# Kernel tuning notes

Hardware: AMD Instinct MI355X
Metric: run time of the kernel (lower is better)

## Reference

```python
import jax, jax.numpy as jnp
import numpy as np

D_MODEL = 2048
N_HEADS = 16
HEAD_DIM = D_MODEL // N_HEADS
BATCH = 2
SEQ = 2048


def rotate_half(x):
    x1, x2 = jnp.split(x, 2, axis=-1)
    return jnp.concatenate((-x2, x1), axis=-1)


def rope_emb(seq_len, head_dim, dtype=jnp.float32):
    inv_freq = 1.0 / (10000.0 ** (jnp.arange(0, head_dim, 2, dtype=jnp.float32) / head_dim))
    t = jnp.arange(seq_len, dtype=jnp.float32)
    freqs = jnp.einsum('i,j->ij', t, inv_freq)            # [S, D/2]
    emb = jnp.concatenate((freqs, freqs), axis=-1)        # [S, D]
    return emb[None, :, None, :].astype(dtype)            # [1, S, 1, D]


def apply_rope(x, emb):
    return x * jnp.cos(emb) + rotate_half(x) * jnp.sin(emb)


def setup_inputs() -> dict:
    key = jax.random.key(0)
    ks = jax.random.split(key, 5)
    s = 1.0 / np.sqrt(D_MODEL)
    return {
        'query': jax.random.normal(ks[0], (BATCH, SEQ, D_MODEL), jnp.float32),
        'Wq': jax.random.normal(ks[1], (D_MODEL, D_MODEL), jnp.float32) * s,
        'Wk': jax.random.normal(ks[2], (D_MODEL, D_MODEL), jnp.float32) * s,
        'Wv': jax.random.normal(ks[3], (D_MODEL, D_MODEL), jnp.float32) * s,
        'Wo': jax.random.normal(ks[4], (D_MODEL, D_MODEL), jnp.float32) * s,
    }


def reference(query, Wq, Wk, Wv, Wo):
    B, S, _ = query.shape
    # QKV projections (nn.Linear: x @ W.T), reshape to [B, S, H, Dh]
    q = (query @ Wq.T).reshape(B, S, N_HEADS, HEAD_DIM)
    k = (query @ Wk.T).reshape(B, S, N_HEADS, HEAD_DIM)
    v = (query @ Wv.T).reshape(B, S, N_HEADS, HEAD_DIM)
    emb = rope_emb(S, HEAD_DIM, q.dtype)
    q = apply_rope(q, emb)
    k = apply_rope(k, emb)
    # causal SDPA
    scale = HEAD_DIM ** -0.5
    scores = jnp.einsum('bqhd,bkhd->bhqk', q, k) * scale  # [B, H, S, S]
    causal = jnp.tril(jnp.ones((S, S), dtype=bool))
    scores = jnp.where(causal, scores, jnp.finfo(scores.dtype).min)
    attn = jax.nn.softmax(scores, axis=-1)
    out = jnp.einsum('bhqk,bkhd->bqhd', attn, v).reshape(B, S, D_MODEL)
    return out @ Wo.T
```

## Files before the change

kernel.cpp:

```cpp
#include <hip/hip_runtime.h>
#include <math.h>

#define BATCH 2
#define SEQ 2048
#define DMODEL 2048
#define NHEADS 16
#define HEADDIM 128
#define MTOT (BATCH * SEQ)
#define QKVLD 6144

typedef __attribute__((ext_vector_type(8))) _Float16 half8;
typedef __attribute__((ext_vector_type(4))) _Float16 half4;
typedef __attribute__((ext_vector_type(4))) float f32x4;

__device__ __forceinline__ void gl_lds16(const void* g, void* l) {
    __builtin_amdgcn_global_load_lds(
        (const __attribute__((address_space(1))) unsigned int*)g,
        (__attribute__((address_space(3))) unsigned int*)l, 16, 0, 0);
}

__global__ __launch_bounds__(256) void f2h_conv(const float* __restrict__ src,
                                                _Float16* __restrict__ dst) {
    size_t i = ((size_t)blockIdx.x * 256 + threadIdx.x) * 8;
    float4 a = *(const float4*)(src + i);
    float4 b = *(const float4*)(src + i + 4);
    union { uint4 u; _Float16 h[8]; } o;
    o.h[0] = (_Float16)a.x; o.h[1] = (_Float16)a.y;
    o.h[2] = (_Float16)a.z; o.h[3] = (_Float16)a.w;
    o.h[4] = (_Float16)b.x; o.h[5] = (_Float16)b.y;
    o.h[6] = (_Float16)b.z; o.h[7] = (_Float16)b.w;
    *(uint4*)(dst + i) = o.u;
}

__global__ __launch_bounds__(256) void f2h3_conv(const float* __restrict__ s0,
                                                 const float* __restrict__ s1,
                                                 const float* __restrict__ s2,
                                                 _Float16* __restrict__ dst) {
    const float* src = (blockIdx.y == 0) ? s0 : (blockIdx.y == 1) ? s1 : s2;
    size_t i = ((size_t)blockIdx.x * 256 + threadIdx.x) * 8;
    float4 a = *(const float4*)(src + i);
    float4 b = *(const float4*)(src + i + 4);
    union { uint4 u; _Float16 h[8]; } o;
    o.h[0] = (_Float16)a.x; o.h[1] = (_Float16)a.y;
    o.h[2] = (_Float16)a.z; o.h[3] = (_Float16)a.w;
    o.h[4] = (_Float16)b.x; o.h[5] = (_Float16)b.y;
    o.h[6] = (_Float16)b.z; o.h[7] = (_Float16)b.w;
    *(uint4*)(dst + (size_t)blockIdx.y * (DMODEL * DMODEL) + i) = o.u;
}

#define SB0  __builtin_amdgcn_sched_barrier(0)
#define BAR  __builtin_amdgcn_s_barrier()
#define VMW4 do { SB0; asm volatile("s_waitcnt vmcnt(4)"); SB0; } while (0)
#define VMW0 do { SB0; asm volatile("s_waitcnt vmcnt(0)"); SB0; } while (0)

template <bool F16OUT>
__global__ __launch_bounds__(512, 2) void gemm8p(const _Float16* __restrict__ A,
                                                 const _Float16* __restrict__ W,
                                                 void* __restrict__ Cout,
                                                 int M, int N, int K) {
    __shared__ __align__(16) _Float16 LAb[2][2][128][64];
    __shared__ __align__(16) _Float16 LBb[2][2][128][64];

    const int tid = threadIdx.x;
    const int lane = tid & 63;
    const int wave = tid >> 6;
    const int quad = lane >> 4;
    const int lcol = lane & 15;
    const int wr = wave >> 2;
    const int wc = wave & 3;
    const int m0 = blockIdx.y * 256;
    const int n0 = blockIdx.x * 256;

    const int srow = tid >> 3;
    const int sc8p = tid & 7;
    const int sc8l = sc8p ^ (srow & 7);

#define STA(BUF, HALF, KT)                                                     \
    do {                                                                       \
        _Pragma("unroll") for (int j = 0; j < 2; j++)                          \
            gl_lds16(A + (size_t)(m0 + (HALF)*128 + j*64 + srow) * K +         \
                         (KT)*64 + sc8l*8,                                     \
                     &LAb[BUF][HALF][j*64 + srow][sc8p*8]);                    \
    } while (0)
#define STB(BUF, HALF, KT)                                                     \
    do {                                                                       \
        _Pragma("unroll") for (int j = 0; j < 2; j++)                          \
            gl_lds16(W + (size_t)(n0 + (HALF)*128 + j*64 + srow) * K +         \
                         (KT)*64 + sc8l*8,                                     \
                     &LBb[BUF][HALF][j*64 + srow][sc8p*8]);                    \
    } while (0)

    auto rdA = [&](int buf, int mf, int ks) -> half8 {
        int R = mf * 16 + lcol;
        return *(const half8*)&LAb[buf][wr][R]
                [(ks * 32 + quad * 8) ^ ((lcol & 7) << 3)];
    };
    auto rdB = [&](int buf, int nf, int ks) -> half8 {
        int R = (wc & 1) * 64 + nf * 16 + lcol;
        return *(const half8*)&LBb[buf][wc >> 1][R]
                [(ks * 32 + quad * 8) ^ ((lcol & 7) << 3)];
    };

    f32x4 acc[8][4];
#pragma unroll
    for (int i = 0; i < 8; i++)
#pragma unroll
        for (int j = 0; j < 4; j++) acc[i][j] = (f32x4){0.f, 0.f, 0.f, 0.f};

#define KTILE4(BUF, S1, S2, S3, S4, W4)                                        \
    {                                                                          \
        half8 a[4][2], b[4][2];                                                \
                         \
        _Pragma("unroll") for (int mf = 0; mf < 4; mf++)                       \
            _Pragma("unroll") for (int ks = 0; ks < 2; ks++)                   \
                a[mf][ks] = rdA(BUF, mf, ks);                                  \
        _Pragma("unroll") for (int nf = 0; nf < 2; nf++)                       \
            _Pragma("unroll") for (int ks = 0; ks < 2; ks++)                   \
                b[nf][ks] = rdB(BUF, nf, ks);                                  \
        S1; SB0; BAR; SB0;                                                     \
        __builtin_amdgcn_s_setprio(1);                                         \
        _Pragma("unroll") for (int ks = 0; ks < 2; ks++)                       \
            _Pragma("unroll") for (int mf = 0; mf < 4; mf++)                   \
                _Pragma("unroll") for (int nf = 0; nf < 2; nf++)               \
                    acc[mf][nf] = __builtin_amdgcn_mfma_f32_16x16x32_f16(      \
                        a[mf][ks], b[nf][ks], acc[mf][nf], 0, 0, 0);           \
        __builtin_amdgcn_s_setprio(0); SB0; BAR; SB0;                          \
                                             \
        _Pragma("unroll") for (int nf = 0; nf < 2; nf++)                       \
            _Pragma("unroll") for (int ks = 0; ks < 2; ks++)                   \
                b[2 + nf][ks] = rdB(BUF, 2 + nf, ks);                          \
        S2; SB0; BAR; SB0;                                                     \
        __builtin_amdgcn_s_setprio(1);                                         \
        _Pragma("unroll") for (int ks = 0; ks < 2; ks++)                       \
            _Pragma("unroll") for (int mf = 0; mf < 4; mf++)                   \
                _Pragma("unroll") for (int nf = 0; nf < 2; nf++)               \
                    acc[mf][2 + nf] = __builtin_amdgcn_mfma_f32_16x16x32_f16(  \
                        a[mf][ks], b[2 + nf][ks], acc[mf][2 + nf], 0, 0, 0);   \
        __builtin_amdgcn_s_setprio(0); SB0; BAR; SB0;                          \
               \
        _Pragma("unroll") for (int mf = 0; mf < 4; mf++)                       \
            _Pragma("unroll") for (int ks = 0; ks < 2; ks++)                   \
                a[mf][ks] = rdA(BUF, 4 + mf, ks);                              \
        S3; SB0; BAR; SB0;                                                     \
        __builtin_amdgcn_s_setprio(1);                                         \
        _Pragma("unroll") for (int ks = 0; ks < 2; ks++)                       \
            _Pragma("unroll") for (int mf = 0; mf < 4; mf++)                   \
                _Pragma("unroll") for (int nf = 0; nf < 2; nf++)               \
                    acc[4 + mf][nf] = __builtin_amdgcn_mfma_f32_16x16x32_f16(  \
                        a[mf][ks], b[nf][ks], acc[4 + mf][nf], 0, 0, 0);       \
        __builtin_amdgcn_s_setprio(0); SB0; BAR; SB0;                          \
              \
        S4; W4; BAR; SB0;                                                      \
        __builtin_amdgcn_s_setprio(1);                                         \
        _Pragma("unroll") for (int ks = 0; ks < 2; ks++)                       \
            _Pragma("unroll") for (int mf = 0; mf < 4; mf++)                   \
                _Pragma("unroll") for (int nf = 0; nf < 2; nf++)               \
                    acc[4 + mf][2 + nf] =                                      \
                        __builtin_amdgcn_mfma_f32_16x16x32_f16(                \
                            a[mf][ks], b[2 + nf][ks], acc[4 + mf][2 + nf],     \
                            0, 0, 0);                                          \
        __builtin_amdgcn_s_setprio(0); SB0; BAR; SB0;                          \
    }

    STB(0, 0, 0); STB(0, 1, 0); STA(0, 0, 0); STA(0, 1, 0);
    STB(1, 0, 1); STB(1, 1, 1);
    VMW4; BAR; SB0;

    const int niter = K >> 7;
    for (int i = 0; i < niter - 1; ++i) {
        const int t0 = 2 * i;
        KTILE4(0, STA(1, 0, t0 + 1), STA(1, 1, t0 + 1),
                  STB(0, 0, t0 + 2), STB(0, 1, t0 + 2), VMW4);
        KTILE4(1, STA(0, 0, t0 + 2), STA(0, 1, t0 + 2),
                  STB(1, 0, t0 + 3), STB(1, 1, t0 + 3), VMW4);
    }
    {
        const int t0 = 2 * (niter - 1);
        KTILE4(0, STA(1, 0, t0 + 1), STA(1, 1, t0 + 1),
                  (void)0, (void)0, VMW0);
        KTILE4(1, (void)0, (void)0, (void)0, (void)0, (void)0);
    }

    float* Cf = (float*)Cout;
    _Float16* Ch = (_Float16*)Cout;
#pragma unroll
    for (int mf = 0; mf < 8; mf++)
#pragma unroll
        for (int nf = 0; nf < 4; nf++)
#pragma unroll
            for (int r = 0; r < 4; r++) {
                size_t row = m0 + wr * 128 + mf * 16 + quad * 4 + r;
                size_t col = n0 + wc * 64 + nf * 16 + lcol;
                if (F16OUT)
                    Ch[row * N + col] = (_Float16)acc[mf][nf][r];
                else
                    Cf[row * N + col] = acc[mf][nf][r];
            }
#undef KTILE4
#undef STA
#undef STB
}

__global__ __launch_bounds__(256) void rope_qk(_Float16* __restrict__ buf) {
    size_t idx = (size_t)blockIdx.x * 256 + threadIdx.x;
    int d = (int)(idx & 63);
    int h = (int)((idx >> 6) & (NHEADS - 1));
    int qk = (int)((idx >> 10) & 1);
    int m = (int)(idx >> 11);
    int s = m & (SEQ - 1);
    float scale = qk ? 1.0f : 0.08838834764831845f;
    float inv = __expf(-(float)d * 0.14391156831212787f);
    float f = (float)s * inv;
    float sn, cs;
    __sincosf(f, &sn, &cs);
    size_t base = (size_t)m * QKVLD + qk * DMODEL + h * HEADDIM + d;
    float x1 = (float)buf[base];
    float x2 = (float)buf[base + 64];
    buf[base]      = (_Float16)((x1 * cs - x2 * sn) * scale);
    buf[base + 64] = (_Float16)((x2 * cs + x1 * sn) * scale);
}

__global__ __launch_bounds__(256) void conv_v_t(const _Float16* __restrict__ src,
                                                _Float16* __restrict__ dst) {
    __shared__ __align__(16) _Float16 T[32][72];
    const int tid = threadIdx.x;
    const int s0 = blockIdx.x * 64;
    const int d0 = blockIdx.y * 32;
    const int bh = blockIdx.z;
    const int b = bh >> 4;
    const int h = bh & 15;

    {
        int s = tid >> 2;
        int d8 = (tid & 3) * 8;
        union { uint4 u; _Float16 hh[8]; } v;
        v.u = *(const uint4*)(src + (size_t)(b * SEQ + s0 + s) * QKVLD +
                              2 * DMODEL + h * HEADDIM + d0 + d8);
#pragma unroll
        for (int j = 0; j < 8; j++) T[d8 + j][s] = v.hh[j];
    }
    __syncthreads();

    int row = tid >> 3;
    int chunk = tid & 7;
    uint4 val = *(const uint4*)&T[row][chunk * 8];
    *(uint4*)(dst + ((size_t)(bh * HEADDIM + d0 + row)) * SEQ + s0 + chunk * 8) = val;
}

__global__ __launch_bounds__(512) void attn_mfma(const _Float16* __restrict__ qkv,
                                                 const _Float16* __restrict__ vtb,
                                                 _Float16* __restrict__ ab) {
    __shared__ __align__(16) _Float16 Ks[64][136];
    __shared__ __align__(16) _Float16 Vts[128][72];
    __shared__ __align__(16) _Float16 Ps[8][16][72];

    const int tid = threadIdx.x;
    const int wave = tid >> 6;
    const int lane = tid & 63;
    const int quad = lane >> 4;
    const int lcol = lane & 15;

    const int h = blockIdx.y;
    const int b = blockIdx.z;
    const int qtA = blockIdx.x;

    const int kr0 = tid >> 4;
    const int ko0 = (tid & 15) * 8;
    const int vr0 = tid >> 3;
    const int vo0 = (tid & 7) * 8;

    const _Float16* kbp = qkv + (size_t)b * SEQ * QKVLD + DMODEL + h * HEADDIM;
    const _Float16* vbp = vtb + ((size_t)(b * NHEADS + h) * HEADDIM) * SEQ;

    uint4 kA, kB, vA, vB;
#define ISSUE_LOAD(kb)                                                        \
    do {                                                                      \
        int _kb = (kb);                                                       \
        kA = *(const uint4*)(kbp + (size_t)(_kb + kr0) * QKVLD + ko0);        \
        kB = *(const uint4*)(kbp + (size_t)(_kb + 32 + kr0) * QKVLD + ko0);   \
        vA = *(const uint4*)(vbp + (size_t)vr0 * SEQ + _kb + vo0);            \
        vB = *(const uint4*)(vbp + (size_t)(vr0 + 64) * SEQ + _kb + vo0);     \
    } while (0)

    ISSUE_LOAD(0);

    for (int ph = 0; ph < 2; ++ph) {
        const int qt = ph ? (15 - qtA) : qtA;
        const int q0 = qt * 128 + wave * 16;
        const int nkt = 2 * qt + 2;

        half8 aq[4];
        {
            const _Float16* qrow =
                qkv + (size_t)(b * SEQ + q0 + lcol) * QKVLD + h * HEADDIM;
#pragma unroll
            for (int st = 0; st < 4; st++)
                aq[st] = *(const half8*)(qrow + quad * 8 + 32 * st);
        }

        f32x4 Of[8];
#pragma unroll
        for (int dt = 0; dt < 8; dt++) Of[dt] = (f32x4){0.f, 0.f, 0.f, 0.f};
        float m_s = -1e30f, l_s = 0.f;

        for (int kt = 0; kt < nkt; ++kt) {
            const int kbase = kt << 6;

            __syncthreads();
            *(uint4*)&Ks[kr0][ko0]        = kA;
            *(uint4*)&Ks[kr0 + 32][ko0]   = kB;
            *(uint4*)&Vts[vr0][vo0]       = vA;
            *(uint4*)&Vts[vr0 + 64][vo0]  = vB;
            __syncthreads();

            if (kt + 1 < nkt)      ISSUE_LOAD((kt + 1) << 6);
            else if (ph == 0)      ISSUE_LOAD(0);

            if (kbase > q0 + 15) continue;

            f32x4 Sc[4];
#pragma unroll
            for (int s = 0; s < 4; s++) {
                Sc[s] = (f32x4){0.f, 0.f, 0.f, 0.f};
#pragma unroll
                for (int st = 0; st < 4; st++) {
                    half8 bk = *(const half8*)&Ks[16 * s + lcol][quad * 8 + 32 * st];
                    Sc[s] = __builtin_amdgcn_mfma_f32_16x16x32_f16(bk, aq[st], Sc[s],
                                                                   0, 0, 0);
                }
            }

            if (kbase + 63 > q0) {
#pragma unroll
                for (int s = 0; s < 4; s++)
#pragma unroll
                    for (int r = 0; r < 4; r++)
                        if (kbase + 16 * s + quad * 4 + r > q0 + lcol)
                            Sc[s][r] = -1e30f;
            }

            float pmax = Sc[0][0];
#pragma unroll
            for (int s = 0; s < 4; s++)
#pragma unroll
                for (int r = 0; r < 4; r++) pmax = fmaxf(pmax, Sc[s][r]);
            pmax = fmaxf(pmax, __shfl_xor(pmax, 16));
            pmax = fmaxf(pmax, __shfl_xor(pmax, 32));

            if (!__all(pmax <= m_s + 5.0f)) {
                float mnew = fmaxf(m_s, pmax);
                float alpha = __expf(m_s - mnew);
                m_s = mnew;
                l_s *= alpha;
                float a0 = __shfl(alpha, quad * 4 + 0);
                float a1 = __shfl(alpha, quad * 4 + 1);
                float a2 = __shfl(alpha, quad * 4 + 2);
                float a3 = __shfl(alpha, quad * 4 + 3);
#pragma unroll
                for (int dt = 0; dt < 8; dt++) {
                    Of[dt][0] *= a0;
                    Of[dt][1] *= a1;
                    Of[dt][2] *= a2;
                    Of[dt][3] *= a3;
                }
            }

            float sum = 0.f;
#pragma unroll
            for (int s = 0; s < 4; s++)
#pragma unroll
                for (int r = 0; r < 4; r++) {
                    float p = __expf(Sc[s][r] - m_s);
                    Sc[s][r] = p;
                    sum += p;
                }
            sum += __shfl_xor(sum, 16);
            sum += __shfl_xor(sum, 32);
            l_s += sum;

#pragma unroll
            for (int s = 0; s < 4; s++) {
                union { half4 v; unsigned long long u; } pk;
                pk.v[0] = (_Float16)Sc[s][0];
                pk.v[1] = (_Float16)Sc[s][1];
                pk.v[2] = (_Float16)Sc[s][2];
                pk.v[3] = (_Float16)Sc[s][3];
                *(half4*)&Ps[wave][lcol][16 * s + 4 * quad] = pk.v;
            }

            half8 ap[2];
#pragma unroll
            for (int st = 0; st < 2; st++)
                ap[st] = *(const half8*)&Ps[wave][lcol][quad * 8 + 32 * st];
#pragma unroll
            for (int dt = 0; dt < 8; dt++) {
#pragma unroll
                for (int st = 0; st < 2; st++) {
                    half8 bv = *(const half8*)&Vts[16 * dt + lcol][quad * 8 + 32 * st];
                    Of[dt] = __builtin_amdgcn_mfma_f32_16x16x32_f16(ap[st], bv, Of[dt],
                                                                    0, 0, 0);
                }
            }
        }

        float invl = 1.f / l_s;
        float i0 = __shfl(invl, quad * 4 + 0);
        float i1 = __shfl(invl, quad * 4 + 1);
        float i2 = __shfl(invl, quad * 4 + 2);
        float i3 = __shfl(invl, quad * 4 + 3);
        _Float16* obase =
            ab + (size_t)(b * SEQ + q0 + quad * 4) * DMODEL + h * HEADDIM;
#pragma unroll
        for (int dt = 0; dt < 8; dt++) {
            obase[(size_t)0 * DMODEL + 16 * dt + lcol] = (_Float16)(Of[dt][0] * i0);
            obase[(size_t)1 * DMODEL + 16 * dt + lcol] = (_Float16)(Of[dt][1] * i1);
            obase[(size_t)2 * DMODEL + 16 * dt + lcol] = (_Float16)(Of[dt][2] * i2);
            obase[(size_t)3 * DMODEL + 16 * dt + lcol] = (_Float16)(Of[dt][3] * i3);
        }
    }
#undef ISSUE_LOAD
}

extern "C" void kernel_launch(void* const* d_in, const int* in_sizes, int n_in,
                              void* d_out, int out_size, void* d_ws, size_t ws_size,
                              hipStream_t stream) {
    const float* query = (const float*)d_in[0];
    const float* Wq = (const float*)d_in[1];
    const float* Wk = (const float*)d_in[2];
    const float* Wv = (const float*)d_in[3];
    const float* Wo = (const float*)d_in[4];
    float* out = (float*)d_out;

    const size_t MB = 1024 * 1024;
    char* w = (char*)d_ws;
    _Float16* xh   = (_Float16*)(w + 0 * MB);
    _Float16* ab   = (_Float16*)(w + 0 * MB);
    _Float16* qkvh = (_Float16*)(w + 16 * MB);
    _Float16* Wh3  = (_Float16*)(w + 64 * MB);
    _Float16* vtb  = (_Float16*)(w + 88 * MB);

    const int convX = (MTOT * DMODEL) / (256 * 8);
    const int convW = (DMODEL * DMODEL) / (256 * 8);
    const int ropeBlocks = (MTOT * 2 * NHEADS * 64) / 256;

    f2h_conv<<<convX, 256, 0, stream>>>(query, xh);
    f2h3_conv<<<dim3(convW, 3), 256, 0, stream>>>(Wq, Wk, Wv, Wh3);

    gemm8p<true><<<dim3(QKVLD / 256, MTOT / 256), 512, 0, stream>>>(
        xh, Wh3, qkvh, MTOT, QKVLD, DMODEL);

    rope_qk<<<ropeBlocks, 256, 0, stream>>>(qkvh);
    conv_v_t<<<dim3(SEQ / 64, HEADDIM / 32, BATCH * NHEADS), 256, 0, stream>>>(qkvh, vtb);

    attn_mfma<<<dim3(8, NHEADS, BATCH), 512, 0, stream>>>(qkvh, vtb, ab);

    f2h_conv<<<convW, 256, 0, stream>>>(Wo, Wh3);
    gemm8p<false><<<dim3(DMODEL / 256, MTOT / 256), 512, 0, stream>>>(
        ab, Wh3, out, MTOT, DMODEL, DMODEL);
}
```

Measured before the change: 439.4 us.

## Merge conversion and RoPE/V-transpose launches, use smaller-tile GEMM for output projection

Combines the input and QKV weight fp16 conversions into one launch, and fuses the RoPE application with the V transpose into a single kernel that processes eight elements per thread. The output projection switches to a simpler 128x128-tile GEMM with 256 threads, so the grid has more blocks than the 256x256 kernel. This is meant to cut launch overhead and improve CU occupancy for the smaller GEMM. The trade-off is that the new GEMM lacks double buffering and writes fp32 output with scalar stores.

```diff
diff --git a/kernel.cpp b/kernel.cpp
--- a/kernel.cpp
+++ b/kernel.cpp
@@ -17,6 +17,37 @@
     __builtin_amdgcn_global_load_lds(
         (const __attribute__((address_space(1))) unsigned int*)g,
         (__attribute__((address_space(3))) unsigned int*)l, 16, 0, 0);
+}
+
+__global__ __launch_bounds__(256) void f2h_multi(const float* __restrict__ query,
+                                                 const float* __restrict__ Wq,
+                                                 const float* __restrict__ Wk,
+                                                 const float* __restrict__ Wv,
+                                                 _Float16* __restrict__ xh,
+                                                 _Float16* __restrict__ Wh3) {
+    const float* src;
+    _Float16* dst;
+    size_t i;
+    int bx = blockIdx.x;
+    if (bx < 4096) {
+        src = query; dst = xh;
+        i = ((size_t)bx * 256 + threadIdx.x) * 8;
+    } else {
+        int wi = bx - 4096;
+        int y = wi >> 11;
+        int off = wi & 2047;
+        src = (y == 0) ? Wq : (y == 1) ? Wk : Wv;
+        dst = Wh3 + (size_t)y * (DMODEL * DMODEL);
+        i = ((size_t)off * 256 + threadIdx.x) * 8;
+    }
+    float4 a = *(const float4*)(src + i);
+    float4 b = *(const float4*)(src + i + 4);
+    union { uint4 u; _Float16 h[8]; } o;
+    o.h[0] = (_Float16)a.x; o.h[1] = (_Float16)a.y;
+    o.h[2] = (_Float16)a.z; o.h[3] = (_Float16)a.w;
+    o.h[4] = (_Float16)b.x; o.h[5] = (_Float16)b.y;
+    o.h[6] = (_Float16)b.z; o.h[7] = (_Float16)b.w;
+    *(uint4*)(dst + i) = o.u;
 }
 
 __global__ __launch_bounds__(256) void f2h_conv(const float* __restrict__ src,
@@ -30,22 +61,6 @@
     o.h[4] = (_Float16)b.x; o.h[5] = (_Float16)b.y;
     o.h[6] = (_Float16)b.z; o.h[7] = (_Float16)b.w;
     *(uint4*)(dst + i) = o.u;
-}
-
-__global__ __launch_bounds__(256) void f2h3_conv(const float* __restrict__ s0,
-                                                 const float* __restrict__ s1,
-                                                 const float* __restrict__ s2,
-                                                 _Float16* __restrict__ dst) {
-    const float* src = (blockIdx.y == 0) ? s0 : (blockIdx.y == 1) ? s1 : s2;
-    size_t i = ((size_t)blockIdx.x * 256 + threadIdx.x) * 8;
-    float4 a = *(const float4*)(src + i);
-    float4 b = *(const float4*)(src + i + 4);
-    union { uint4 u; _Float16 h[8]; } o;
-    o.h[0] = (_Float16)a.x; o.h[1] = (_Float16)a.y;
-    o.h[2] = (_Float16)a.z; o.h[3] = (_Float16)a.w;
-    o.h[4] = (_Float16)b.x; o.h[5] = (_Float16)b.y;
-    o.h[6] = (_Float16)b.z; o.h[7] = (_Float16)b.w;
-    *(uint4*)(dst + (size_t)blockIdx.y * (DMODEL * DMODEL) + i) = o.u;
 }
 
 #define SB0  __builtin_amdgcn_sched_barrier(0)
@@ -110,7 +125,6 @@
 #define KTILE4(BUF, S1, S2, S3, S4, W4)                                        \
     {                                                                          \
         half8 a[4][2], b[4][2];                                                \
-                         \
         _Pragma("unroll") for (int mf = 0; mf < 4; mf++)                       \
             _Pragma("unroll") for (int ks = 0; ks < 2; ks++)                   \
                 a[mf][ks] = rdA(BUF, mf, ks);                                  \
@@ -125,7 +139,6 @@
                     acc[mf][nf] = __builtin_amdgcn_mfma_f32_16x16x32_f16(      \
                         a[mf][ks], b[nf][ks], acc[mf][nf], 0, 0, 0);           \
         __builtin_amdgcn_s_setprio(0); SB0; BAR; SB0;                          \
-                                             \
         _Pragma("unroll") for (int nf = 0; nf < 2; nf++)                       \
             _Pragma("unroll") for (int ks = 0; ks < 2; ks++)                   \
                 b[2 + nf][ks] = rdB(BUF, 2 + nf, ks);                          \
@@ -137,7 +150,6 @@
                     acc[mf][2 + nf] = __builtin_amdgcn_mfma_f32_16x16x32_f16(  \
                         a[mf][ks], b[2 + nf][ks], acc[mf][2 + nf], 0, 0, 0);   \
         __builtin_amdgcn_s_setprio(0); SB0; BAR; SB0;                          \
-               \
         _Pragma("unroll") for (int mf = 0; mf < 4; mf++)                       \
             _Pragma("unroll") for (int ks = 0; ks < 2; ks++)                   \
                 a[mf][ks] = rdA(BUF, 4 + mf, ks);                              \
@@ -149,7 +161,6 @@
                     acc[4 + mf][nf] = __builtin_amdgcn_mfma_f32_16x16x32_f16(  \
                         a[mf][ks], b[nf][ks], acc[4 + mf][nf], 0, 0, 0);       \
         __builtin_amdgcn_s_setprio(0); SB0; BAR; SB0;                          \
-              \
         S4; W4; BAR; SB0;                                                      \
         __builtin_amdgcn_s_setprio(1);                                         \
         _Pragma("unroll") for (int ks = 0; ks < 2; ks++)                       \
@@ -201,50 +212,132 @@
 #undef STB
 }
 
-__global__ __launch_bounds__(256) void rope_qk(_Float16* __restrict__ buf) {
-    size_t idx = (size_t)blockIdx.x * 256 + threadIdx.x;
-    int d = (int)(idx & 63);
-    int h = (int)((idx >> 6) & (NHEADS - 1));
-    int qk = (int)((idx >> 10) & 1);
-    int m = (int)(idx >> 11);
-    int s = m & (SEQ - 1);
-    float scale = qk ? 1.0f : 0.08838834764831845f;
-    float inv = __expf(-(float)d * 0.14391156831212787f);
-    float f = (float)s * inv;
-    float sn, cs;
-    __sincosf(f, &sn, &cs);
-    size_t base = (size_t)m * QKVLD + qk * DMODEL + h * HEADDIM + d;
-    float x1 = (float)buf[base];
-    float x2 = (float)buf[base + 64];
-    buf[base]      = (_Float16)((x1 * cs - x2 * sn) * scale);
-    buf[base + 64] = (_Float16)((x2 * cs + x1 * sn) * scale);
-}
-
-__global__ __launch_bounds__(256) void conv_v_t(const _Float16* __restrict__ src,
-                                                _Float16* __restrict__ dst) {
+template <bool F16OUT>
+__global__ __launch_bounds__(256) void gemm_h(const _Float16* __restrict__ A,
+                                              const _Float16* __restrict__ W,
+                                              void* __restrict__ Cout,
+                                              int M, int N, int K) {
+    __shared__ __align__(16) _Float16 As[128 * 32];
+    __shared__ __align__(16) _Float16 Bs[128 * 32];
+
+    const int tid = threadIdx.x;
+    const int wv = tid >> 6;
+    const int ln = tid & 63;
+    const int quad = ln >> 4;
+    const int lcol = ln & 15;
+    const int m0 = blockIdx.y * 128;
+    const int n0 = blockIdx.x * 128;
+    const int wm = (wv >> 1) * 64;
+    const int wn = (wv & 1) * 64;
+
+    const int srow = ln >> 2;
+    const int kblk = (ln & 3) * 8;
+
+    f32x4 acc[4][4];
+#pragma unroll
+    for (int i = 0; i < 4; i++)
+#pragma unroll
+        for (int j = 0; j < 4; j++) acc[i][j] = (f32x4){0.f, 0.f, 0.f, 0.f};
+
+    for (int k0 = 0; k0 < K; k0 += 32) {
+        __syncthreads();
+#pragma unroll
+        for (int j = 0; j < 2; j++) {
+            int r = wv * 32 + j * 16 + srow;
+            gl_lds16(A + (size_t)(m0 + r) * K + k0 + kblk, &As[r * 32 + kblk]);
+            gl_lds16(W + (size_t)(n0 + r) * K + k0 + kblk, &Bs[r * 32 + kblk]);
+        }
+        __syncthreads();
+
+        half8 af[4], bf[4];
+#pragma unroll
+        for (int ms = 0; ms < 4; ms++)
+            af[ms] = *(const half8*)&As[(wm + ms * 16 + lcol) * 32 + quad * 8];
+#pragma unroll
+        for (int ns = 0; ns < 4; ns++)
+            bf[ns] = *(const half8*)&Bs[(wn + ns * 16 + lcol) * 32 + quad * 8];
+#pragma unroll
+        for (int ms = 0; ms < 4; ms++)
+#pragma unroll
+            for (int ns = 0; ns < 4; ns++)
+                acc[ms][ns] = __builtin_amdgcn_mfma_f32_16x16x32_f16(
+                    af[ms], bf[ns], acc[ms][ns], 0, 0, 0);
+    }
+
+    float* Cf = (float*)Cout;
+    _Float16* Ch = (_Float16*)Cout;
+#pragma unroll
+    for (int ms = 0; ms < 4; ms++)
+#pragma unroll
+        for (int ns = 0; ns < 4; ns++)
+#pragma unroll
+            for (int r = 0; r < 4; r++) {
+                size_t row = m0 + wm + ms * 16 + quad * 4 + r;
+                size_t col = n0 + wn + ns * 16 + lcol;
+                if (F16OUT)
+                    Ch[row * N + col] = (_Float16)acc[ms][ns][r];
+                else
+                    Cf[row * N + col] = acc[ms][ns][r];
+            }
+}
+
+__global__ __launch_bounds__(256) void prep_kv(_Float16* __restrict__ qkv,
+                                               _Float16* __restrict__ vtb) {
     __shared__ __align__(16) _Float16 T[32][72];
+    int bx = blockIdx.x;
     const int tid = threadIdx.x;
-    const int s0 = blockIdx.x * 64;
-    const int d0 = blockIdx.y * 32;
-    const int bh = blockIdx.z;
-    const int b = bh >> 4;
-    const int h = bh & 15;
-
-    {
-        int s = tid >> 2;
-        int d8 = (tid & 3) * 8;
-        union { uint4 u; _Float16 hh[8]; } v;
-        v.u = *(const uint4*)(src + (size_t)(b * SEQ + s0 + s) * QKVLD +
-                              2 * DMODEL + h * HEADDIM + d0 + d8);
-#pragma unroll
-        for (int j = 0; j < 8; j++) T[d8 + j][s] = v.hh[j];
-    }
-    __syncthreads();
-
-    int row = tid >> 3;
-    int chunk = tid & 7;
-    uint4 val = *(const uint4*)&T[row][chunk * 8];
-    *(uint4*)(dst + ((size_t)(bh * HEADDIM + d0 + row)) * SEQ + s0 + chunk * 8) = val;
+
+    if (bx < 4096) {
+        size_t idx = (size_t)bx * 256 + tid;
+        int chunk = (int)(idx & 7);
+        int h = (int)((idx >> 3) & (NHEADS - 1));
+        int qk = (int)((idx >> 7) & 1);
+        int m = (int)(idx >> 8);
+        int s = m & (SEQ - 1);
+        float scale = qk ? 1.0f : 0.08838834764831845f;
+        int d8 = chunk * 8;
+
+        size_t base = (size_t)m * QKVLD + qk * DMODEL + h * HEADDIM + d8;
+        union { uint4 u; _Float16 hh[8]; } u0, u1, o0, o1;
+        u0.u = *(const uint4*)(qkv + base);
+        u1.u = *(const uint4*)(qkv + base + 64);
+#pragma unroll
+        for (int j = 0; j < 8; j++) {
+            float inv = __expf(-(float)(d8 + j) * 0.14391156831212787f);
+            float f = (float)s * inv;
+            float sn, cs;
+            __sincosf(f, &sn, &cs);
+            float x1 = (float)u0.hh[j];
+            float x2 = (float)u1.hh[j];
+            o0.hh[j] = (_Float16)((x1 * cs - x2 * sn) * scale);
+            o1.hh[j] = (_Float16)((x2 * cs + x1 * sn) * scale);
+        }
+        *(uint4*)(qkv + base) = o0.u;
+        *(uint4*)(qkv + base + 64) = o1.u;
+    } else {
+        int v = bx - 4096;
+        const int s0 = (v & 31) * 64;
+        const int d0 = ((v >> 5) & 3) * 32;
+        const int bh = v >> 7;
+        const int b = bh >> 4;
+        const int h = bh & 15;
+
+        {
+            int s = tid >> 2;
+            int d8 = (tid & 3) * 8;
+            union { uint4 u; _Float16 hh[8]; } vv;
+            vv.u = *(const uint4*)(qkv + (size_t)(b * SEQ + s0 + s) * QKVLD +
+                                   2 * DMODEL + h * HEADDIM + d0 + d8);
+#pragma unroll
+            for (int j = 0; j < 8; j++) T[d8 + j][s] = vv.hh[j];
+        }
+        __syncthreads();
+
+        int row = tid >> 3;
+        int chunk = tid & 7;
+        uint4 val = *(const uint4*)&T[row][chunk * 8];
+        *(uint4*)(vtb + ((size_t)(bh * HEADDIM + d0 + row)) * SEQ + s0 + chunk * 8) = val;
+    }
 }
 
 __global__ __launch_bounds__(512) void attn_mfma(const _Float16* __restrict__ qkv,
@@ -380,12 +473,10 @@
 
 #pragma unroll
             for (int s = 0; s < 4; s++) {
-                union { half4 v; unsigned long long u; } pk;
-                pk.v[0] = (_Float16)Sc[s][0];
-                pk.v[1] = (_Float16)Sc[s][1];
-                pk.v[2] = (_Float16)Sc[s][2];
-                pk.v[3] = (_Float16)Sc[s][3];
-                *(half4*)&Ps[wave][lcol][16 * s + 4 * quad] = pk.v;
+                half4 pk;
+                pk[0] = (_Float16)Sc[s][0]; pk[1] = (_Float16)Sc[s][1];
+                pk[2] = (_Float16)Sc[s][2]; pk[3] = (_Float16)Sc[s][3];
+                *(half4*)&Ps[wave][lcol][16 * s + 4 * quad] = pk;
             }
 
             half8 ap[2];
@@ -439,22 +530,18 @@
     _Float16* Wh3  = (_Float16*)(w + 64 * MB);
     _Float16* vtb  = (_Float16*)(w + 88 * MB);
 
-    const int convX = (MTOT * DMODEL) / (256 * 8);
     const int convW = (DMODEL * DMODEL) / (256 * 8);
-    const int ropeBlocks = (MTOT * 2 * NHEADS * 64) / 256;
-
-    f2h_conv<<<convX, 256, 0, stream>>>(query, xh);
-    f2h3_conv<<<dim3(convW, 3), 256, 0, stream>>>(Wq, Wk, Wv, Wh3);
+
+    f2h_multi<<<4096 + 3 * 2048, 256, 0, stream>>>(query, Wq, Wk, Wv, xh, Wh3);
 
     gemm8p<true><<<dim3(QKVLD / 256, MTOT / 256), 512, 0, stream>>>(
         xh, Wh3, qkvh, MTOT, QKVLD, DMODEL);
 
-    rope_qk<<<ropeBlocks, 256, 0, stream>>>(qkvh);
-    conv_v_t<<<dim3(SEQ / 64, HEADDIM / 32, BATCH * NHEADS), 256, 0, stream>>>(qkvh, vtb);
+    prep_kv<<<4096 + 4096, 256, 0, stream>>>(qkvh, vtb);
 
     attn_mfma<<<dim3(8, NHEADS, BATCH), 512, 0, stream>>>(qkvh, vtb, ab);
 
     f2h_conv<<<convW, 256, 0, stream>>>(Wo, Wh3);
-    gemm8p<false><<<dim3(DMODEL / 256, MTOT / 256), 512, 0, stream>>>(
+    gemm_h<false><<<dim3(DMODEL / 128, MTOT / 128), 256, 0, stream>>>(
         ab, Wh3, out, MTOT, DMODEL, DMODEL);
 }
```

After: 419.7 us. -4.5%, faster.
